# Kernel optimization log

Measured on AMD Instinct MI355X. Metric: run time of the kernel, lower is better.

## Reference

```python
import jax, jax.numpy as jnp
import numpy as np

Nc, Nt, B, L = 24, 1024, 32, 24
D = Nt // 4          # 256 encoder_output_dim
C16 = 16 * Nc        # 384 per-channel linears
H8 = 8 * Nc          # 192 LSTM hidden
WS = 0.02            # weight scale for numerical stability


def setup_inputs() -> dict:
    key = jax.random.key(0)
    ctr = [0]
    def nk():
        ctr[0] += 1
        return jax.random.fold_in(key, ctr[0])
    def rn(shape, s=WS):
        return jax.random.normal(nk(), shape, dtype=jnp.float32) * s
    def ru(shape):
        return jax.random.uniform(nk(), shape, dtype=jnp.float32)
    inp = {}
    inp["x"] = rn((B, 1, Nc, Nt), 1.0)
    inp["eps"] = rn((B, C16, L), 1.0)
    inp["sconv_w"] = rn((2 * Nc, 1, Nc, 1)); inp["sconv_b"] = rn((2 * Nc,))
    inp["tconv1_w"] = rn((4 * Nc, 2 * Nc, 1, 16)); inp["tconv1_b"] = rn((4 * Nc,))
    inp["tconv2_w"] = rn((8 * Nc, 4 * Nc, 1, 16)); inp["tconv2_b"] = rn((8 * Nc,))
    for i, c in ((1, 2 * Nc), (2, 4 * Nc), (3, 8 * Nc), (4, 4 * Nc), (5, 2 * Nc), (6, 2 * Nc)):
        inp[f"bn{i}_g"] = ru((c,)); inp[f"bn{i}_b"] = rn((c,))
        inp[f"bn{i}_m"] = jnp.zeros((c,), jnp.float32); inp[f"bn{i}_v"] = jnp.ones((c,), jnp.float32)
        inp[f"a{i}"] = ru((1,))
    for d in ("f", "b"):
        inp[f"w_ih_{d}"] = rn((4 * H8, H8)); inp[f"w_hh_{d}"] = rn((4 * H8, H8))
        inp[f"b_ih_{d}"] = rn((4 * H8,)); inp[f"b_hh_{d}"] = rn((4 * H8,))
    inp["mu_w"] = rn((C16, L, D)); inp["mu_b"] = rn((C16, L))
    inp["lv_w"] = rn((C16, L, D)); inp["lv_b"] = rn((C16, L))
    inp["dec_w"] = rn((C16, D, L)); inp["dec_b"] = rn((C16, D))
    inp["dconv1_w"] = rn((16 * Nc, 4 * Nc, 1, 16)); inp["dconv1_b"] = rn((4 * Nc,))
    inp["dconv2_w"] = rn((8 * Nc, 2 * Nc, 1, 16)); inp["dconv2_b"] = rn((2 * Nc,))
    inp["sdconv_w"] = rn((4 * Nc, 2 * Nc, Nc, 1)); inp["sdconv_b"] = rn((2 * Nc,))
    inp["fconv_w"] = rn((1, 2 * Nc, 1, 1)); inp["fconv_b"] = rn((1,))
    return inp


def _bn(x, g, b, m, v):
    scale = (g * jax.lax.rsqrt(v + 1e-5))[None, :, None, None]
    return (x - m[None, :, None, None]) * scale + b[None, :, None, None]


def _prelu(x, a):
    return jnp.where(x >= 0, x, a * x)


def _conv(x, w, b, stride, pad):
    y = jax.lax.conv_general_dilated(x, w, stride, pad,
                                     dimension_numbers=("NCHW", "OIHW", "NCHW"))
    return y + b[None, :, None, None]


def _convT(x, w, b, stride, pad, opad):
    # w in PyTorch ConvTranspose2d layout (Cin, Cout, kH, kW)
    w2 = jnp.flip(jnp.transpose(w, (1, 0, 2, 3)), (2, 3))
    kH, kW = w.shape[2], w.shape[3]
    padding = ((kH - 1 - pad[0], kH - 1 - pad[0] + opad[0]),
               (kW - 1 - pad[1], kW - 1 - pad[1] + opad[1]))
    y = jax.lax.conv_general_dilated(x, w2, (1, 1), padding, lhs_dilation=stride,
                                     dimension_numbers=("NCHW", "OIHW", "NCHW"))
    return y + b[None, :, None, None]


def _lstm_dir(xs, w_ih, w_hh, b_ih, b_hh, reverse):
    # xs: (T, B, In); PyTorch gate order i, f, g, o
    gx = jnp.einsum("tbi,gi->tbg", xs, w_ih) + (b_ih + b_hh)
    Bb, Hh = xs.shape[1], w_hh.shape[1]
    def step(carry, gt):
        h, c = carry
        gates = gt + h @ w_hh.T
        i, f, g, o = jnp.split(gates, 4, axis=-1)
        c = jax.nn.sigmoid(f) * c + jax.nn.sigmoid(i) * jnp.tanh(g)
        h = jax.nn.sigmoid(o) * jnp.tanh(c)
        return (h, c), h
    init = (jnp.zeros((Bb, Hh), xs.dtype), jnp.zeros((Bb, Hh), xs.dtype))
    _, hs = jax.lax.scan(step, init, gx, reverse=reverse)
    return hs  # (T, B, H), aligned with input time order


def _forward(p):
    # Encoder (dropout = identity, BN in eval mode)
    x1 = _prelu(_bn(_conv(p["x"], p["sconv_w"], p["sconv_b"], (Nc, 1), ((0, 0), (0, 0))),
                    p["bn1_g"], p["bn1_b"], p["bn1_m"], p["bn1_v"]), p["a1"])   # (B,2Nc,1,Nt)
    x2 = _prelu(_bn(_conv(x1, p["tconv1_w"], p["tconv1_b"], (1, 2), ((0, 0), (7, 7))),
                    p["bn2_g"], p["bn2_b"], p["bn2_m"], p["bn2_v"]), p["a2"])   # (B,4Nc,1,Nt/2)
    x3 = _prelu(_bn(_conv(x2, p["tconv2_w"], p["tconv2_b"], (1, 2), ((0, 0), (7, 7))),
                    p["bn3_g"], p["bn3_b"], p["bn3_m"], p["bn3_v"]), p["a3"])   # (B,8Nc,1,Nt/4)
    x3s = jnp.transpose(x3[:, :, 0, :], (2, 0, 1))                              # (T,B,8Nc)
    hf = _lstm_dir(x3s, p["w_ih_f"], p["w_hh_f"], p["b_ih_f"], p["b_hh_f"], False)
    hb = _lstm_dir(x3s, p["w_ih_b"], p["w_hh_b"], p["b_ih_b"], p["b_hh_b"], True)
    h = jnp.concatenate([hf, hb], axis=-1)                                      # (T,B,16Nc)
    h = h.reshape(D, x3.shape[0], H8, 2).mean(-1)                               # AvgPool1d(k=2) over feature dim
    tr = jnp.transpose(h, (1, 2, 0))                                            # (B,8Nc,T)
    e0 = jnp.concatenate([tr, x3[:, :, 0, :]], axis=1)                          # (B,16Nc,T=D)
    # 16*Nc per-channel Linears fused as batched GEMMs
    mu = jnp.einsum("bcd,cld->bcl", e0, p["mu_w"]) + p["mu_b"]                  # (B,384,L)
    logvar = jnp.einsum("bcd,cld->bcl", e0, p["lv_w"]) + p["lv_b"]
    z = mu + p["eps"] * jnp.exp(0.5 * logvar)
    x4 = (jnp.einsum("bcl,cdl->bcd", z, p["dec_w"]) + p["dec_b"])[:, :, None, :]  # (B,384,1,D)
    # Decoder (Nt%4==0 and Nt%2==0 -> output_padding 0)
    u1 = _prelu(_bn(_convT(x4, p["dconv1_w"], p["dconv1_b"], (1, 2), (0, 7), (0, 0)),
                    p["bn4_g"], p["bn4_b"], p["bn4_m"], p["bn4_v"]), p["a4"])   # (B,4Nc,1,Nt/2)
    e1 = jnp.concatenate([u1, x2], axis=1)                                      # (B,8Nc,1,Nt/2)
    u2 = _prelu(_bn(_convT(e1, p["dconv2_w"], p["dconv2_b"], (1, 2), (0, 7), (0, 0)),
                    p["bn5_g"], p["bn5_b"], p["bn5_m"], p["bn5_v"]), p["a5"])   # (B,2Nc,1,Nt)
    e2 = jnp.concatenate([u2, x1], axis=1)                                      # (B,4Nc,1,Nt)
    u3 = _prelu(_bn(_convT(e2, p["sdconv_w"], p["sdconv_b"], (Nc, 1), (0, 0), (0, 0)),
                    p["bn6_g"], p["bn6_b"], p["bn6_m"], p["bn6_v"]), p["a6"])   # (B,2Nc,Nc,Nt)
    out = _conv(u3, p["fconv_w"], p["fconv_b"], (1, 1), ((0, 0), (0, 0)))       # (B,1,Nc,Nt)
    return out, mu, logvar


def reference(x, eps, sconv_w, sconv_b, tconv1_w, tconv1_b, tconv2_w, tconv2_b,
              bn1_g, bn1_b, bn1_m, bn1_v, a1, bn2_g, bn2_b, bn2_m, bn2_v, a2,
              bn3_g, bn3_b, bn3_m, bn3_v, a3, bn4_g, bn4_b, bn4_m, bn4_v, a4,
              bn5_g, bn5_b, bn5_m, bn5_v, a5, bn6_g, bn6_b, bn6_m, bn6_v, a6,
              w_ih_f, w_hh_f, b_ih_f, b_hh_f, w_ih_b, w_hh_b, b_ih_b, b_hh_b,
              mu_w, mu_b, lv_w, lv_b, dec_w, dec_b,
              dconv1_w, dconv1_b, dconv2_w, dconv2_b, sdconv_w, sdconv_b,
              fconv_w, fconv_b):
    p = dict(locals())
    return _forward(p)
```

## Files before the change

### kernel.cpp

```cpp
#include <hip/hip_runtime.h>
#include <cstdint>

#define DI __device__ __forceinline__

typedef __attribute__((ext_vector_type(8))) short s8v;
typedef __attribute__((ext_vector_type(4))) float f4v;

DI float sigmoidf_(float x) {
    x = fminf(fmaxf(x, -30.f), 30.f);
    return 1.f / (1.f + __expf(-x));
}
DI float tanhf_(float x) {
    x = fminf(fmaxf(x, -15.f), 15.f);
    float e = __expf(2.f * x);
    return (e - 1.f) / (e + 1.f);
}
DI uint32_t f2bf(float f) {
    uint32_t u = __float_as_uint(f);
    return (u + 0x7fffu + ((u >> 16) & 1u)) >> 16;
}

__global__ __launch_bounds__(256) void k_prep(
    const float* wihf, const float* wihb, const float* whhf, const float* whhb,
    const float* bihf, const float* bhhf, const float* bihb, const float* bhhb,
    const float* sdw,
    float* wihT, uint32_t* wfrag, float* bsum, float* wsdT)
{
    int i = blockIdx.x * 256 + threadIdx.x;
    if (i < 294912) {
        int d = i / 147456, r = i % 147456;
        int ii = r / 768, g = r % 768;
        const float* w = d ? wihb : wihf;
        wihT[i] = w[g * 192 + ii];
        return;
    }
    int j = i - 294912;
    if (j < 147456) {
        int d = j / 73728, r = j % 73728;
        int w = r / 6144, r2 = r % 6144;
        int tau = r2 / 1536, r3 = r2 % 1536;
        int kt = r3 / 256, r4 = r3 % 256;
        int lane = r4 / 4, jp = r4 % 4;
        int n = 16 * (w + 12 * tau) + (lane & 15);
        int k0 = kt * 32 + (lane >> 4) * 8 + jp * 2;
        const float* whh = d ? whhb : whhf;
        uint32_t lo = f2bf(whh[n * 192 + k0]);
        uint32_t hi = f2bf(whh[n * 192 + k0 + 1]);
        wfrag[j] = lo | (hi << 16);
        return;
    }
    int k = j - 147456;
    if (k < 1536) {
        int d = k / 768, g = k % 768;
        bsum[k] = d ? (bihb[g] + bhhb[g]) : (bihf[g] + bhhf[g]);
        return;
    }
    int l = k - 1536;
    if (l < 110592) {
        int h = l / 4608, rem = l % 4608;
        int co = rem / 96, ci = rem % 96;
        wsdT[l] = sdw[(ci * 48 + co) * 24 + h];
    }
}

__global__ __launch_bounds__(256) void k_sconv(
    const float* __restrict__ x, const float* __restrict__ w, const float* __restrict__ bias,
    const float* g, const float* bb, const float* m, const float* v, const float* a,
    float* __restrict__ x1)
{
    int t = blockIdx.x * 256 + threadIdx.x;
    int co = blockIdx.y;
    int b = blockIdx.z;
    const float* xb = x + (size_t)b * 24 * 1024 + t;
    float acc = bias[co];
#pragma unroll
    for (int h = 0; h < 24; ++h) acc = fmaf(xb[h * 1024], w[co * 24 + h], acc);
    float sc = g[co] * rsqrtf(v[co] + 1e-5f);
    float y = (acc - m[co]) * sc + bb[co];
    float al = a[0];
    y = y >= 0.f ? y : al * y;
    x1[((size_t)b * 48 + co) * 1024 + t] = y;
}

template<int CI, int CO, int WOUT, int BSTR>
__global__ __launch_bounds__(256) void k_tconv(
    const float* __restrict__ xin, const float* __restrict__ w, const float* __restrict__ bias,
    const float* g, const float* bb, const float* m, const float* v, const float* a,
    float* __restrict__ out)
{
    const int WIN = WOUT * 2;
    __shared__ float XL[CI][144];
    int tid = threadIdx.x;
    int w0 = blockIdx.x * 64;
    int b = blockIdx.z;
    for (int idx = tid; idx < CI * 144; idx += 256) {
        int ci = idx / 144, p = idx % 144;
        int gp = 2 * w0 - 7 + p;
        XL[ci][p] = (gp >= 0 && gp < WIN) ? xin[((size_t)b * CI + ci) * WIN + gp] : 0.f;
    }
    __syncthreads();
    int tw = tid & 63, cg = tid >> 6;
    int co0 = blockIdx.y * 16 + cg * 4;
    co0 = __builtin_amdgcn_readfirstlane(co0);
    const float* wb = w + (size_t)co0 * CI * 16;
    float acc[4] = {bias[co0], bias[co0 + 1], bias[co0 + 2], bias[co0 + 3]};
    for (int ci = 0; ci < CI; ++ci) {
#pragma unroll
        for (int k = 0; k < 16; ++k) {
            float xv = XL[ci][2 * tw + k];
            acc[0] = fmaf(xv, wb[(0 * CI + ci) * 16 + k], acc[0]);
            acc[1] = fmaf(xv, wb[(1 * CI + ci) * 16 + k], acc[1]);
            acc[2] = fmaf(xv, wb[(2 * CI + ci) * 16 + k], acc[2]);
            acc[3] = fmaf(xv, wb[(3 * CI + ci) * 16 + k], acc[3]);
        }
    }
    float al = a[0];
#pragma unroll
    for (int r = 0; r < 4; ++r) {
        int co = co0 + r;
        float sc = g[co] * rsqrtf(v[co] + 1e-5f);
        float y = (acc[r] - m[co]) * sc + bb[co];
        y = y >= 0.f ? y : al * y;
        out[((size_t)b * BSTR + co) * WOUT + w0 + tw] = y;
    }
}

__global__ __launch_bounds__(256) void k_x3s(const float* __restrict__ e0, float* __restrict__ x3s)
{
    __shared__ float tl[64 * 193];
    int t0 = blockIdx.x * 64, b = blockIdx.y;
    int tid = threadIdx.x;
    for (int idx = tid; idx < 192 * 64; idx += 256) {
        int i = idx >> 6, tt = idx & 63;
        tl[tt * 193 + i] = e0[((size_t)b * 384 + 192 + i) * 256 + t0 + tt];
    }
    __syncthreads();
    for (int idx = tid; idx < 64 * 192; idx += 256) {
        int tt = idx / 192, ii = idx % 192;
        x3s[((size_t)(t0 + tt) * 32 + b) * 192 + ii] = tl[tt * 193 + ii];
    }
}

__global__ __launch_bounds__(256) void k_gemm(
    const float* __restrict__ A, const float* __restrict__ Bm,
    const float* __restrict__ bias, float* __restrict__ C)
{
    __shared__ float AL[64 * 17];
    __shared__ float BL[16 * 68];
    int tid = threadIdx.x;
    int n0 = blockIdx.x * 64, m0 = blockIdx.y * 64;
    int tx = tid & 15, ty = tid >> 4;
    float4 cc[4] = {};
    for (int k0 = 0; k0 < 192; k0 += 16) {
        for (int idx = tid; idx < 1024; idx += 256) {
            int r = idx >> 4, c = idx & 15;
            AL[r * 17 + c] = A[(size_t)(m0 + r) * 192 + k0 + c];
        }
        for (int idx = tid; idx < 1024; idx += 256) {
            int kk = idx >> 6, jj = idx & 63;
            BL[kk * 68 + jj] = Bm[(size_t)(k0 + kk) * 768 + n0 + jj];
        }
        __syncthreads();
#pragma unroll
        for (int kk = 0; kk < 16; ++kk) {
            float4 b4 = *(const float4*)&BL[kk * 68 + tx * 4];
            float a0 = AL[(ty * 4 + 0) * 17 + kk];
            float a1 = AL[(ty * 4 + 1) * 17 + kk];
            float a2 = AL[(ty * 4 + 2) * 17 + kk];
            float a3 = AL[(ty * 4 + 3) * 17 + kk];
            cc[0].x = fmaf(a0, b4.x, cc[0].x); cc[0].y = fmaf(a0, b4.y, cc[0].y);
            cc[0].z = fmaf(a0, b4.z, cc[0].z); cc[0].w = fmaf(a0, b4.w, cc[0].w);
            cc[1].x = fmaf(a1, b4.x, cc[1].x); cc[1].y = fmaf(a1, b4.y, cc[1].y);
            cc[1].z = fmaf(a1, b4.z, cc[1].z); cc[1].w = fmaf(a1, b4.w, cc[1].w);
            cc[2].x = fmaf(a2, b4.x, cc[2].x); cc[2].y = fmaf(a2, b4.y, cc[2].y);
            cc[2].z = fmaf(a2, b4.z, cc[2].z); cc[2].w = fmaf(a2, b4.w, cc[2].w);
            cc[3].x = fmaf(a3, b4.x, cc[3].x); cc[3].y = fmaf(a3, b4.y, cc[3].y);
            cc[3].z = fmaf(a3, b4.z, cc[3].z); cc[3].w = fmaf(a3, b4.w, cc[3].w);
        }
        __syncthreads();
    }
    float4 bs = *(const float4*)&bias[n0 + tx * 4];
#pragma unroll
    for (int i = 0; i < 4; ++i) {
        float4 r = cc[i];
        r.x += bs.x; r.y += bs.y; r.z += bs.z; r.w += bs.w;
        *(float4*)&C[(size_t)(m0 + ty * 4 + i) * 768 + n0 + tx * 4] = r;
    }
}

__global__ __launch_bounds__(768, 3) void k_lstm_mfma(
    const float* __restrict__ gx, const short* __restrict__ wfrag, float* __restrict__ e0)
{
    int bid = blockIdx.x;
    int d = bid >> 1;
    int b0 = (bid & 1) * 16;
    int tid = threadIdx.x;
    int w = tid >> 6;
    int l = tid & 63;
    int lm = l & 15, lq = l >> 4;

    __shared__ __align__(16) short Hf[3072];

    s8v Bf[4][6];
    {
        const short* wb = wfrag + (size_t)((d * 12 + w) * 4) * 3072 + (size_t)l * 8;
#pragma unroll
        for (int tau = 0; tau < 4; ++tau)
#pragma unroll
            for (int kt = 0; kt < 6; ++kt)
                Bf[tau][kt] = *(const s8v*)(wb + (tau * 6 + kt) * 512);
    }
    for (int i2 = tid; i2 < 1536; i2 += 768) ((uint32_t*)Hf)[i2] = 0u;

    float c[4] = {0.f, 0.f, 0.f, 0.f};

    const float* gxb = gx + (size_t)d * 6291456 + (size_t)(b0 + lq * 4) * 768 + w * 16 + lm;

    float pre[4][4];
    {
        int t0 = d ? 255 : 0;
        const float* gp = gxb + (size_t)t0 * 24576;
#pragma unroll
        for (int tau = 0; tau < 4; ++tau)
#pragma unroll
            for (int r = 0; r < 4; ++r)
                pre[tau][r] = gp[r * 768 + tau * 192];
    }

    int j = w * 16 + lm;
    int kt_j = j >> 5, kg_j = (j >> 3) & 3, off_j = j & 7;
    int hw_u32 = (kt_j * 512 + (kg_j * 16 + lq * 4) * 8 + (off_j & ~1)) >> 1;
    float* e0t = e0 + (size_t)d * 24576 + (size_t)(b0 + lq * 4) * 98304 + (j >> 1) * 256;

    __syncthreads();

    for (int s = 0; s < 256; ++s) {
        int t = d ? 255 - s : s;
        f4v acc[4];
#pragma unroll
        for (int tau = 0; tau < 4; ++tau) {
            f4v a0 = {pre[tau][0], pre[tau][1], pre[tau][2], pre[tau][3]};
            acc[tau] = a0;
        }
        if (s < 255) {
            int tn = d ? 254 - s : s + 1;
            const float* gp = gxb + (size_t)tn * 24576;
#pragma unroll
            for (int tau = 0; tau < 4; ++tau)
#pragma unroll
                for (int r = 0; r < 4; ++r)
                    pre[tau][r] = gp[r * 768 + tau * 192];
        }
#pragma unroll
        for (int kt = 0; kt < 6; ++kt) {
            s8v A = *(const s8v*)&Hf[kt * 512 + l * 8];
            acc[0] = __builtin_amdgcn_mfma_f32_16x16x32_bf16(A, Bf[0][kt], acc[0], 0, 0, 0);
            acc[1] = __builtin_amdgcn_mfma_f32_16x16x32_bf16(A, Bf[1][kt], acc[1], 0, 0, 0);
            acc[2] = __builtin_amdgcn_mfma_f32_16x16x32_bf16(A, Bf[2][kt], acc[2], 0, 0, 0);
            acc[3] = __builtin_amdgcn_mfma_f32_16x16x32_bf16(A, Bf[3][kt], acc[3], 0, 0, 0);
        }
        float hv[4];
#pragma unroll
        for (int r = 0; r < 4; ++r) {
            float ig = sigmoidf_(acc[0][r]);
            float fg = sigmoidf_(acc[1][r]);
            float gg = tanhf_(acc[2][r]);
            float og = sigmoidf_(acc[3][r]);
            c[r] = fmaf(fg, c[r], ig * gg);
            hv[r] = og * tanhf_(c[r]);
        }
        float hp[4];
#pragma unroll
        for (int r = 0; r < 4; ++r) hp[r] = __shfl_xor(hv[r], 1);
        __syncthreads();
        if ((lm & 1) == 0) {
#pragma unroll
            for (int r = 0; r < 4; ++r) {
                ((uint32_t*)Hf)[hw_u32 + r * 4] = f2bf(hv[r]) | (f2bf(hp[r]) << 16);
                e0t[(size_t)r * 98304 + t] = 0.5f * (hv[r] + hp[r]);
            }
        }
        __syncthreads();
    }
}

__global__ __launch_bounds__(256) void k_muz(
    const float* __restrict__ e0, const float* __restrict__ muw, const float* __restrict__ mub,
    const float* __restrict__ lvw, const float* __restrict__ lvb, const float* __restrict__ eps,
    float* __restrict__ mu_out, float* __restrict__ lv_out, float* __restrict__ z)
{
    int c = blockIdx.x;
    int tid = threadIdx.x;
    __shared__ float eL[32 * 257];
    __shared__ float gL[48 * 33];
    for (int idx = tid; idx < 8192; idx += 256) {
        int b = idx >> 8, dd = idx & 255;
        eL[b * 257 + dd] = e0[((size_t)b * 384 + c) * 256 + dd];
    }
    __syncthreads();
    for (int rep = 0; rep < 6; ++rep) {
        int task = rep * 256 + tid;
        int b = task & 31, r = task >> 5;
        const float* row = (r < 24) ? (muw + ((size_t)c * 24 + r) * 256)
                                    : (lvw + ((size_t)c * 24 + (r - 24)) * 256);
        float acc = 0.f;
#pragma unroll 4
        for (int dd = 0; dd < 256; ++dd) acc = fmaf(eL[b * 257 + dd], row[dd], acc);
        acc += (r < 24) ? mub[c * 24 + r] : lvb[c * 24 + (r - 24)];
        gL[r * 33 + b] = acc;
    }
    __syncthreads();
    for (int rep = 0; rep < 3; ++rep) {
        int task = rep * 256 + tid;
        int b = task / 24, l = task % 24;
        float muv = gL[l * 33 + b], lvv = gL[(24 + l) * 33 + b];
        size_t oi = ((size_t)b * 384 + c) * 24 + l;
        mu_out[oi] = muv;
        lv_out[oi] = lvv;
        z[oi] = fmaf(eps[oi], __expf(0.5f * lvv), muv);
    }
}

__global__ __launch_bounds__(256) void k_dec(
    const float* __restrict__ z, const float* __restrict__ dw, const float* __restrict__ db,
    float* __restrict__ x4)
{
    int c = blockIdx.x, tid = threadIdx.x;
    __shared__ float zL[32 * 25];
    __shared__ float WdL[256 * 25];
    for (int idx = tid; idx < 768; idx += 256) {
        int b = idx / 24, l = idx % 24;
        zL[b * 25 + l] = z[((size_t)b * 384 + c) * 24 + l];
    }
    for (int idx = tid; idx < 6144; idx += 256) {
        int dd = idx / 24, l = idx % 24;
        WdL[dd * 25 + l] = dw[((size_t)c * 256 + dd) * 24 + l];
    }
    __syncthreads();
    for (int rep = 0; rep < 32; ++rep) {
        int task = rep * 256 + tid;
        int b = task >> 8, dd = task & 255;
        float acc = db[c * 256 + dd];
#pragma unroll
        for (int l = 0; l < 24; ++l) acc = fmaf(zL[b * 25 + l], WdL[dd * 25 + l], acc);
        x4[((size_t)b * 384 + c) * 256 + dd] = acc;
    }
}

template<int CI, int CO, int WIN, int SPLIT>
__global__ __launch_bounds__(256) void k_convT(
    const float* __restrict__ in1, const float* __restrict__ in2, const float* __restrict__ w,
    const float* __restrict__ bias, const float* g, const float* bb, const float* m,
    const float* v, const float* a, float* __restrict__ out)
{
    const int WOUT = WIN * 2;
    constexpr int R = CO / 16;
    __shared__ float XL[8 * 41];
    __shared__ float WL[8 * CO * 18];
    int tid = threadIdx.x;
    int w0 = blockIdx.x * 64, b = blockIdx.z;
    int u0 = w0 >> 1;
    int wq = tid & 15, cq = tid >> 4;
    float acc[4][R];
#pragma unroll
    for (int i = 0; i < 4; ++i)
#pragma unroll
        for (int r = 0; r < R; ++r) acc[i][r] = 0.f;

    for (int ci0 = 0; ci0 < CI; ci0 += 8) {
        __syncthreads();
        for (int idx = tid; idx < 320; idx += 256) {
            int ci = idx / 40, p = idx % 40;
            int dpos = u0 - 4 + p;
            int cig = ci0 + ci;
            float val = 0.f;
            if (dpos >= 0 && dpos < WIN)
                val = (cig < SPLIT) ? in1[((size_t)b * SPLIT + cig) * WIN + dpos]
                                    : in2[((size_t)b * (CI - SPLIT) + (cig - SPLIT)) * WIN + dpos];
            XL[ci * 41 + p] = val;
        }
        for (int idx = tid; idx < 8 * CO * 16; idx += 256) {
            int ci = idx / (CO * 16), rem = idx % (CO * 16);
            int co = rem / 16, k = rem & 15;
            WL[(ci * CO + co) * 18 + k] = w[((size_t)(ci0 + ci) * CO + co) * 16 + k];
        }
        __syncthreads();
        for (int ci = 0; ci < 8; ++ci) {
            float xr[10];
#pragma unroll
            for (int p = 0; p < 10; ++p) xr[p] = XL[ci * 41 + 2 * wq + p];
#pragma unroll
            for (int j = 0; j < 8; ++j) {
                float xa = xr[7 - j];
                float xb = xr[8 - j];
                float xc = xr[9 - j];
#pragma unroll
                for (int r = 0; r < R; ++r) {
                    float2 wv = *(const float2*)&WL[(ci * CO + cq * R + r) * 18 + 2 * j];
                    acc[0][r] = fmaf(xa, wv.y, acc[0][r]);
                    acc[1][r] = fmaf(xb, wv.x, acc[1][r]);
                    acc[2][r] = fmaf(xb, wv.y, acc[2][r]);
                    acc[3][r] = fmaf(xc, wv.x, acc[3][r]);
                }
            }
        }
    }
    float al = a[0];
#pragma unroll
    for (int r = 0; r < R; ++r) {
        int co = cq * R + r;
        float sc = g[co] * rsqrtf(v[co] + 1e-5f);
        float bi = bias[co], mm = m[co], be = bb[co];
        float4 yv;
        float* yf = (float*)&yv;
#pragma unroll
        for (int i = 0; i < 4; ++i) {
            float y = (acc[i][r] + bi - mm) * sc + be;
            yf[i] = y >= 0.f ? y : al * y;
        }
        *(float4*)&out[((size_t)b * CO + co) * WOUT + w0 + wq * 4] = yv;
    }
}

__global__ __launch_bounds__(256) void k_final(
    const float* __restrict__ u2, const float* __restrict__ x1, const float* __restrict__ wsdT,
    const float* __restrict__ sdb, const float* g, const float* bb, const float* m,
    const float* v, const float* a, const float* fcw, const float* fcb, float* __restrict__ out)
{
    __shared__ float e2L[64 * 100];
    __shared__ float WL[48 * 100];
    __shared__ float red[64 * 17];
    int tid = threadIdx.x;
    int t0 = blockIdx.x * 64, h = blockIdx.y, b = blockIdx.z;
    for (int idx = tid; idx < 6144; idx += 256) {
        int ci = idx >> 6, tt = idx & 63;
        float vv = (ci < 48) ? u2[((size_t)b * 48 + ci) * 1024 + t0 + tt]
                             : x1[((size_t)b * 48 + (ci - 48)) * 1024 + t0 + tt];
        e2L[tt * 100 + ci] = vv;
    }
    for (int idx = tid; idx < 4608; idx += 256) {
        WL[(idx / 96) * 100 + (idx % 96)] = wsdT[(size_t)h * 4608 + idx];
    }
    __syncthreads();
    int tx = tid & 15, ty = tid >> 4;
    float accv[4][3] = {};
    for (int c4 = 0; c4 < 24; ++c4) {
        float4 e4[4], w4[3];
#pragma unroll
        for (int i = 0; i < 4; ++i) e4[i] = *(const float4*)&e2L[(tx + 16 * i) * 100 + c4 * 4];
#pragma unroll
        for (int r = 0; r < 3; ++r) w4[r] = *(const float4*)&WL[(ty * 3 + r) * 100 + c4 * 4];
#pragma unroll
        for (int i = 0; i < 4; ++i)
#pragma unroll
            for (int r = 0; r < 3; ++r) {
                accv[i][r] = fmaf(e4[i].x, w4[r].x, accv[i][r]);
                accv[i][r] = fmaf(e4[i].y, w4[r].y, accv[i][r]);
                accv[i][r] = fmaf(e4[i].z, w4[r].z, accv[i][r]);
                accv[i][r] = fmaf(e4[i].w, w4[r].w, accv[i][r]);
            }
    }
    float al = a[0];
    float psum[4] = {};
#pragma unroll
    for (int r = 0; r < 3; ++r) {
        int co = ty * 3 + r;
        float sc = g[co] * rsqrtf(v[co] + 1e-5f);
        float fw = fcw[co], bi = sdb[co], mm = m[co], be = bb[co];
#pragma unroll
        for (int i = 0; i < 4; ++i) {
            float y = (accv[i][r] + bi - mm) * sc + be;
            y = y >= 0.f ? y : al * y;
            psum[i] = fmaf(fw, y, psum[i]);
        }
    }
#pragma unroll
    for (int i = 0; i < 4; ++i) red[(i * 16 + tx) * 17 + ty] = psum[i];
    __syncthreads();
    if (tid < 64) {
        float s = fcb[0];
#pragma unroll
        for (int y2 = 0; y2 < 16; ++y2) s += red[tid * 17 + y2];
        out[((size_t)b * 24 + h) * 1024 + t0 + tid] = s;
    }
}

extern "C" void kernel_launch(void* const* d_in, const int* in_sizes, int n_in,
                              void* d_out, int out_size, void* d_ws, size_t ws_size,
                              hipStream_t stream)
{
    (void)in_sizes; (void)n_in; (void)out_size; (void)ws_size;
    const float* x        = (const float*)d_in[0];
    const float* eps      = (const float*)d_in[1];
    const float* sconv_w  = (const float*)d_in[2];
    const float* sconv_b  = (const float*)d_in[3];
    const float* tconv1_w = (const float*)d_in[4];
    const float* tconv1_b = (const float*)d_in[5];
    const float* tconv2_w = (const float*)d_in[6];
    const float* tconv2_b = (const float*)d_in[7];
    const float *bn1g=(const float*)d_in[8],  *bn1b=(const float*)d_in[9],  *bn1m=(const float*)d_in[10], *bn1v=(const float*)d_in[11], *a1=(const float*)d_in[12];
    const float *bn2g=(const float*)d_in[13], *bn2b=(const float*)d_in[14], *bn2m=(const float*)d_in[15], *bn2v=(const float*)d_in[16], *a2=(const float*)d_in[17];
    const float *bn3g=(const float*)d_in[18], *bn3b=(const float*)d_in[19], *bn3m=(const float*)d_in[20], *bn3v=(const float*)d_in[21], *a3=(const float*)d_in[22];
    const float *bn4g=(const float*)d_in[23], *bn4b=(const float*)d_in[24], *bn4m=(const float*)d_in[25], *bn4v=(const float*)d_in[26], *a4=(const float*)d_in[27];
    const float *bn5g=(const float*)d_in[28], *bn5b=(const float*)d_in[29], *bn5m=(const float*)d_in[30], *bn5v=(const float*)d_in[31], *a5=(const float*)d_in[32];
    const float *bn6g=(const float*)d_in[33], *bn6b=(const float*)d_in[34], *bn6m=(const float*)d_in[35], *bn6v=(const float*)d_in[36], *a6=(const float*)d_in[37];
    const float *wihf=(const float*)d_in[38], *whhf=(const float*)d_in[39], *bihf=(const float*)d_in[40], *bhhf=(const float*)d_in[41];
    const float *wihb=(const float*)d_in[42], *whhb=(const float*)d_in[43], *bihb=(const float*)d_in[44], *bhhb=(const float*)d_in[45];
    const float *mu_w=(const float*)d_in[46], *mu_b=(const float*)d_in[47];
    const float *lv_w=(const float*)d_in[48], *lv_b=(const float*)d_in[49];
    const float *dec_w=(const float*)d_in[50], *dec_b=(const float*)d_in[51];
    const float *dconv1_w=(const float*)d_in[52], *dconv1_b=(const float*)d_in[53];
    const float *dconv2_w=(const float*)d_in[54], *dconv2_b=(const float*)d_in[55];
    const float *sdconv_w=(const float*)d_in[56], *sdconv_b=(const float*)d_in[57];
    const float *fconv_w=(const float*)d_in[58], *fconv_b=(const float*)d_in[59];

    float* ws = (float*)d_ws;
    float* x1   = ws + 0;
    float* x2   = ws + 1572864;
    float* e0   = ws + 3145728;
    float* x3s  = ws + 6291456;
    float* wihT = ws + 7864320;
    uint32_t* wfrag = (uint32_t*)(ws + 8159232);
    float* bsum = ws + 8306688;
    float* gx   = ws + 8308736;
    float* z    = ws + 8308736;
    float* x4   = ws + 8603648;
    float* u1   = ws + 11749376;
    float* u2   = ws + 13322240;
    float* wsdT = ws + 20891648;

    float* out0 = (float*)d_out;
    float* muo  = out0 + 786432;
    float* lvo  = muo + 294912;

    k_prep<<<2166, 256, 0, stream>>>(wihf, wihb, whhf, whhb, bihf, bhhf, bihb, bhhb,
                                     sdconv_w, wihT, wfrag, bsum, wsdT);
    k_sconv<<<dim3(4, 48, 32), 256, 0, stream>>>(x, sconv_w, sconv_b, bn1g, bn1b, bn1m, bn1v, a1, x1);
    k_tconv<48, 96, 512, 96><<<dim3(8, 6, 32), 256, 0, stream>>>(
        x1, tconv1_w, tconv1_b, bn2g, bn2b, bn2m, bn2v, a2, x2);
    k_tconv<96, 192, 256, 384><<<dim3(4, 12, 32), 256, 0, stream>>>(
        x2, tconv2_w, tconv2_b, bn3g, bn3b, bn3m, bn3v, a3, e0 + 49152);
    k_x3s<<<dim3(4, 32), 256, 0, stream>>>(e0, x3s);
    k_gemm<<<dim3(12, 128), 256, 0, stream>>>(x3s, wihT, bsum, gx);
    k_gemm<<<dim3(12, 128), 256, 0, stream>>>(x3s, wihT + 147456, bsum + 768, gx + 6291456);
    k_lstm_mfma<<<4, 768, 0, stream>>>(gx, (const short*)wfrag, e0);
    k_muz<<<384, 256, 0, stream>>>(e0, mu_w, mu_b, lv_w, lv_b, eps, muo, lvo, z);
    k_dec<<<384, 256, 0, stream>>>(z, dec_w, dec_b, x4);
    k_convT<384, 96, 256, 384><<<dim3(8, 1, 32), 256, 0, stream>>>(
        x4, x4, dconv1_w, dconv1_b, bn4g, bn4b, bn4m, bn4v, a4, u1);
    k_convT<192, 48, 512, 96><<<dim3(16, 1, 32), 256, 0, stream>>>(
        u1, x2, dconv2_w, dconv2_b, bn5g, bn5b, bn5m, bn5v, a5, u2);
    k_final<<<dim3(16, 24, 32), 256, 0, stream>>>(
        u2, x1, wsdT, sdconv_b, bn6g, bn6b, bn6m, bn6v, a6, fconv_w, fconv_b, out0);
}
```

Before: 2.035 ms.

## Double-buffer LSTM hidden state, defer output writes, split convT channels

```diff
diff --git a/kernel.cpp b/kernel.cpp
--- a/kernel.cpp
+++ b/kernel.cpp
@@ -7,18 +7,17 @@
 typedef __attribute__((ext_vector_type(4))) float f4v;
 
 DI float sigmoidf_(float x) {
-    x = fminf(fmaxf(x, -30.f), 30.f);
-    return 1.f / (1.f + __expf(-x));
+    return __builtin_amdgcn_rcpf(1.f + __expf(-x));
 }
 DI float tanhf_(float x) {
-    x = fminf(fmaxf(x, -15.f), 15.f);
-    float e = __expf(2.f * x);
-    return (e - 1.f) / (e + 1.f);
+    return fmaf(-2.f, __builtin_amdgcn_rcpf(1.f + __expf(2.f * x)), 1.f);
 }
 DI uint32_t f2bf(float f) {
     uint32_t u = __float_as_uint(f);
     return (u + 0x7fffu + ((u >> 16) & 1u)) >> 16;
 }
+DI float bflo(uint32_t u) { return __uint_as_float(u << 16); }
+DI float bfhi(uint32_t u) { return __uint_as_float(u & 0xffff0000u); }
 
 __global__ __launch_bounds__(256) void k_prep(
     const float* wihf, const float* wihb, const float* whhf, const float* whhb,
@@ -188,9 +187,13 @@
     }
 }
 
-__global__ __launch_bounds__(768, 3) void k_lstm_mfma(
-    const float* __restrict__ gx, const short* __restrict__ wfrag, float* __restrict__ e0)
-{
+__global__ __launch_bounds__(768) void k_lstm_mfma(
+    const float* __restrict__ gx, const short* __restrict__ wfrag,
+    float* __restrict__ htmp)
+{
+    extern __shared__ short wB[];
+    __shared__ __align__(16) short Hf[2][3072];
+
     int bid = blockIdx.x;
     int d = bid >> 1;
     int b0 = (bid & 1) * 16;
@@ -199,23 +202,26 @@
     int l = tid & 63;
     int lm = l & 15, lq = l >> 4;
 
-    __shared__ __align__(16) short Hf[3072];
-
-    s8v Bf[4][6];
+    s8v Bf[2][6];
     {
-        const short* wb = wfrag + (size_t)((d * 12 + w) * 4) * 3072 + (size_t)l * 8;
-#pragma unroll
-        for (int tau = 0; tau < 4; ++tau)
+        const short* wb = wfrag + ((size_t)(d * 12 + w) * 4) * 3072 + (size_t)l * 8;
+#pragma unroll
+        for (int tau = 0; tau < 2; ++tau)
 #pragma unroll
             for (int kt = 0; kt < 6; ++kt)
                 Bf[tau][kt] = *(const s8v*)(wb + (tau * 6 + kt) * 512);
-    }
-    for (int i2 = tid; i2 < 1536; i2 += 768) ((uint32_t*)Hf)[i2] = 0u;
-
-    float c[4] = {0.f, 0.f, 0.f, 0.f};
+#pragma unroll
+        for (int tau = 2; tau < 4; ++tau)
+#pragma unroll
+            for (int kt = 0; kt < 6; ++kt)
+                *(uint4*)&wB[(((w * 2 + (tau - 2)) * 6 + kt) * 64 + l) * 8] =
+                    *(const uint4*)(wb + (tau * 6 + kt) * 512);
+    }
+    for (int i2 = tid; i2 < 1536; i2 += 768) ((uint32_t*)Hf[0])[i2] = 0u;
+
+    float c4[4] = {0.f, 0.f, 0.f, 0.f};
 
     const float* gxb = gx + (size_t)d * 6291456 + (size_t)(b0 + lq * 4) * 768 + w * 16 + lm;
-
     float pre[4][4];
     {
         int t0 = d ? 255 : 0;
@@ -230,12 +236,13 @@
     int j = w * 16 + lm;
     int kt_j = j >> 5, kg_j = (j >> 3) & 3, off_j = j & 7;
     int hw_u32 = (kt_j * 512 + (kg_j * 16 + lq * 4) * 8 + (off_j & ~1)) >> 1;
-    float* e0t = e0 + (size_t)d * 24576 + (size_t)(b0 + lq * 4) * 98304 + (j >> 1) * 256;
+    float* hbase = htmp + ((size_t)d * 256 * 32 + b0 + lm) * 96 + lq * 4;
 
     __syncthreads();
 
     for (int s = 0; s < 256; ++s) {
         int t = d ? 255 - s : s;
+        int p = s & 1;
         f4v acc[4];
 #pragma unroll
         for (int tau = 0; tau < 4; ++tau) {
@@ -251,13 +258,27 @@
                 for (int r = 0; r < 4; ++r)
                     pre[tau][r] = gp[r * 768 + tau * 192];
         }
+        bool dost = (w == 0) && (s > 0);
+        int tprev = d ? t + 1 : t - 1;
+        float* hst = hbase + (size_t)tprev * 3072;
 #pragma unroll
         for (int kt = 0; kt < 6; ++kt) {
-            s8v A = *(const s8v*)&Hf[kt * 512 + l * 8];
+            s8v A = *(const s8v*)&Hf[p][kt * 512 + l * 8];
+            if (dost) {
+                const uint32_t* au = (const uint32_t*)&A;
+                float4 pv;
+                pv.x = 0.5f * (bflo(au[0]) + bfhi(au[0]));
+                pv.y = 0.5f * (bflo(au[1]) + bfhi(au[1]));
+                pv.z = 0.5f * (bflo(au[2]) + bfhi(au[2]));
+                pv.w = 0.5f * (bflo(au[3]) + bfhi(au[3]));
+                *(float4*)&hst[kt * 16] = pv;
+            }
+            s8v B2 = *(const s8v*)&wB[(((w * 2 + 0) * 6 + kt) * 64 + l) * 8];
+            s8v B3 = *(const s8v*)&wB[(((w * 2 + 1) * 6 + kt) * 64 + l) * 8];
             acc[0] = __builtin_amdgcn_mfma_f32_16x16x32_bf16(A, Bf[0][kt], acc[0], 0, 0, 0);
             acc[1] = __builtin_amdgcn_mfma_f32_16x16x32_bf16(A, Bf[1][kt], acc[1], 0, 0, 0);
-            acc[2] = __builtin_amdgcn_mfma_f32_16x16x32_bf16(A, Bf[2][kt], acc[2], 0, 0, 0);
-            acc[3] = __builtin_amdgcn_mfma_f32_16x16x32_bf16(A, Bf[3][kt], acc[3], 0, 0, 0);
+            acc[2] = __builtin_amdgcn_mfma_f32_16x16x32_bf16(A, B2, acc[2], 0, 0, 0);
+            acc[3] = __builtin_amdgcn_mfma_f32_16x16x32_bf16(A, B3, acc[3], 0, 0, 0);
         }
         float hv[4];
 #pragma unroll
@@ -266,21 +287,52 @@
             float fg = sigmoidf_(acc[1][r]);
             float gg = tanhf_(acc[2][r]);
             float og = sigmoidf_(acc[3][r]);
-            c[r] = fmaf(fg, c[r], ig * gg);
-            hv[r] = og * tanhf_(c[r]);
+            c4[r] = fmaf(fg, c4[r], ig * gg);
+            hv[r] = og * tanhf_(c4[r]);
         }
         float hp[4];
 #pragma unroll
         for (int r = 0; r < 4; ++r) hp[r] = __shfl_xor(hv[r], 1);
+        if ((lm & 1) == 0) {
+            uint32_t* dst = (uint32_t*)Hf[p ^ 1];
+#pragma unroll
+            for (int r = 0; r < 4; ++r)
+                dst[hw_u32 + r * 4] = f2bf(hv[r]) | (f2bf(hp[r]) << 16);
+        }
         __syncthreads();
-        if ((lm & 1) == 0) {
-#pragma unroll
-            for (int r = 0; r < 4; ++r) {
-                ((uint32_t*)Hf)[hw_u32 + r * 4] = f2bf(hv[r]) | (f2bf(hp[r]) << 16);
-                e0t[(size_t)r * 98304 + t] = 0.5f * (hv[r] + hp[r]);
-            }
-        }
-        __syncthreads();
+    }
+    if (w == 0) {
+        int tlast = d ? 0 : 255;
+        float* hst = hbase + (size_t)tlast * 3072;
+#pragma unroll
+        for (int kt = 0; kt < 6; ++kt) {
+            s8v A = *(const s8v*)&Hf[0][kt * 512 + l * 8];
+            const uint32_t* au = (const uint32_t*)&A;
+            float4 pv;
+            pv.x = 0.5f * (bflo(au[0]) + bfhi(au[0]));
+            pv.y = 0.5f * (bflo(au[1]) + bfhi(au[1]));
+            pv.z = 0.5f * (bflo(au[2]) + bfhi(au[2]));
+            pv.w = 0.5f * (bflo(au[3]) + bfhi(au[3]));
+            *(float4*)&hst[kt * 16] = pv;
+        }
+    }
+}
+
+__global__ __launch_bounds__(256) void k_hT(const float* __restrict__ htmp, float* __restrict__ e0)
+{
+    __shared__ float tl[96 * 65];
+    int t0 = blockIdx.x * 64;
+    int b = blockIdx.y;
+    int d = blockIdx.z;
+    int tid = threadIdx.x;
+    for (int idx = tid; idx < 6144; idx += 256) {
+        int tt = idx / 96, jp = idx % 96;
+        tl[jp * 65 + tt] = htmp[(((size_t)d * 256 + t0 + tt) * 32 + b) * 96 + jp];
+    }
+    __syncthreads();
+    for (int idx = tid; idx < 6144; idx += 256) {
+        int jp = idx >> 6, tt = idx & 63;
+        e0[((size_t)b * 384 + d * 96 + jp) * 256 + t0 + tt] = tl[jp * 65 + tt];
     }
 }
 
@@ -347,7 +399,7 @@
     }
 }
 
-template<int CI, int CO, int WIN, int SPLIT>
+template<int CI, int CO, int WIN, int SPLIT, int COFULL>
 __global__ __launch_bounds__(256) void k_convT(
     const float* __restrict__ in1, const float* __restrict__ in2, const float* __restrict__ w,
     const float* __restrict__ bias, const float* g, const float* bb, const float* m,
@@ -359,6 +411,7 @@
     __shared__ float WL[8 * CO * 18];
     int tid = threadIdx.x;
     int w0 = blockIdx.x * 64, b = blockIdx.z;
+    int cb = blockIdx.y * CO;
     int u0 = w0 >> 1;
     int wq = tid & 15, cq = tid >> 4;
     float acc[4][R];
@@ -382,7 +435,7 @@
         for (int idx = tid; idx < 8 * CO * 16; idx += 256) {
             int ci = idx / (CO * 16), rem = idx % (CO * 16);
             int co = rem / 16, k = rem & 15;
-            WL[(ci * CO + co) * 18 + k] = w[((size_t)(ci0 + ci) * CO + co) * 16 + k];
+            WL[(ci * CO + co) * 18 + k] = w[((size_t)(ci0 + ci) * COFULL + cb + co) * 16 + k];
         }
         __syncthreads();
         for (int ci = 0; ci < 8; ++ci) {
@@ -408,7 +461,7 @@
     float al = a[0];
 #pragma unroll
     for (int r = 0; r < R; ++r) {
-        int co = cq * R + r;
+        int co = cb + cq * R + r;
         float sc = g[co] * rsqrtf(v[co] + 1e-5f);
         float bi = bias[co], mm = m[co], be = bb[co];
         float4 yv;
@@ -418,7 +471,7 @@
             float y = (acc[i][r] + bi - mm) * sc + be;
             yf[i] = y >= 0.f ? y : al * y;
         }
-        *(float4*)&out[((size_t)b * CO + co) * WOUT + w0 + wq * 4] = yv;
+        *(float4*)&out[((size_t)b * COFULL + co) * WOUT + w0 + wq * 4] = yv;
     }
 }
 
@@ -519,6 +572,7 @@
     float* x2   = ws + 1572864;
     float* e0   = ws + 3145728;
     float* x3s  = ws + 6291456;
+    float* htmp = ws + 6291456;
     float* wihT = ws + 7864320;
     uint32_t* wfrag = (uint32_t*)(ws + 8159232);
     float* bsum = ws + 8306688;
@@ -532,6 +586,9 @@
     float* out0 = (float*)d_out;
     float* muo  = out0 + 786432;
     float* lvo  = muo + 294912;
+
+    (void)hipFuncSetAttribute((const void*)k_lstm_mfma,
+                              hipFuncAttributeMaxDynamicSharedMemorySize, 147456);
 
     k_prep<<<2166, 256, 0, stream>>>(wihf, wihb, whhf, whhb, bihf, bhhf, bihb, bhhb,
                                      sdconv_w, wihT, wfrag, bsum, wsdT);
@@ -543,12 +600,13 @@
     k_x3s<<<dim3(4, 32), 256, 0, stream>>>(e0, x3s);
     k_gemm<<<dim3(12, 128), 256, 0, stream>>>(x3s, wihT, bsum, gx);
     k_gemm<<<dim3(12, 128), 256, 0, stream>>>(x3s, wihT + 147456, bsum + 768, gx + 6291456);
-    k_lstm_mfma<<<4, 768, 0, stream>>>(gx, (const short*)wfrag, e0);
+    k_lstm_mfma<<<4, 768, 147456, stream>>>(gx, (const short*)wfrag, htmp);
+    k_hT<<<dim3(4, 32, 2), 256, 0, stream>>>(htmp, e0);
     k_muz<<<384, 256, 0, stream>>>(e0, mu_w, mu_b, lv_w, lv_b, eps, muo, lvo, z);
     k_dec<<<384, 256, 0, stream>>>(z, dec_w, dec_b, x4);
-    k_convT<384, 96, 256, 384><<<dim3(8, 1, 32), 256, 0, stream>>>(
+    k_convT<384, 48, 256, 384, 96><<<dim3(8, 2, 32), 256, 0, stream>>>(
         x4, x4, dconv1_w, dconv1_b, bn4g, bn4b, bn4m, bn4v, a4, u1);
-    k_convT<192, 48, 512, 96><<<dim3(16, 1, 32), 256, 0, stream>>>(
+    k_convT<192, 48, 512, 96, 48><<<dim3(16, 1, 32), 256, 0, stream>>>(
         u1, x2, dconv2_w, dconv2_b, bn5g, bn5b, bn5m, bn5v, a5, u2);
     k_final<<<dim3(16, 24, 32), 256, 0, stream>>>(
         u2, x1, wsdT, sdconv_b, bn6g, bn6b, bn6m, bn6v, a6, fconv_w, fconv_b, out0);
```

Measured after the change: 1.708 ms. -16.1%, faster.
